# Kernel tuning notes

Measured on AMD Instinct MI355X. Metric: run time of the kernel, lower is better.

The kernel has to match this reference:

```python
import jax, jax.numpy as jnp
import numpy as np

K = 2            # top-k experts
TEMPERATURE = 1.0
EPS = 1e-9


def setup_inputs() -> dict:
    key = jax.random.key(0)
    k1, k2 = jax.random.split(key)
    B, S, D = 4, 4096, 4096
    G, E = 4, 64
    x = jax.random.normal(k1, (B, S, D), dtype=jnp.float32)
    # stacked gate weights, one [E, D] Linear weight per gate head
    W = jax.random.normal(k2, (G, E, D), dtype=jnp.float32) * 0.02
    return {"x": x, "W": W}


def reference(x, W):
    # per-head logits over experts: [B, S, G, E]; jitter disabled (eval / jitter_noise=0)
    logits = jnp.einsum('bsd,ged->bsge', x, W) * (1.0 / TEMPERATURE)
    probs = jax.nn.softmax(logits, axis=-1)          # softmax per head
    probs_full = probs.mean(axis=2)                  # consensus over heads: [B, S, E]
    topk_vals, idx = jax.lax.top_k(probs_full, K)    # sorted descending, matches aten.topk
    den = jnp.sum(topk_vals, axis=-1, keepdims=True)
    scores = topk_vals / jnp.maximum(den, EPS)       # clamp_min(den, 1e-9)
    pf = jax.lax.stop_gradient(probs_full)           # aux stats under no_grad
    importance = pf.mean(axis=(0, 1))                # [E]
    load = (pf > 0.0).astype(pf.dtype).mean(axis=(0, 1))  # [E]
    return idx, scores, probs_full, importance, load
```

## Files before the change

### kernel.cpp

```cpp
#include <hip/hip_runtime.h>

typedef _Float16 f16x8  __attribute__((ext_vector_type(8)));
typedef float    f32x4  __attribute__((ext_vector_type(4)));
typedef float    f32x16 __attribute__((ext_vector_type(16)));

#define MROWS 16384
#define NCOLS 256
#define KDIM  4096
#define BM    128
#define BK    32
#define LDA   34

#define OUT_SCORES 32768
#define OUT_PF     65536
#define OUT_IMP    1114112
#define OUT_LOAD   1114176

#define FIN_BLOCKS 1024

__global__ __launch_bounds__(256) void wprep(const float* __restrict__ W,
                                             _Float16* __restrict__ wfHi,
                                             _Float16* __restrict__ wfLo) {
    int t  = blockIdx.x * 256 + threadIdx.x;
    int n  = t >> 9;
    int k8 = t & 511;
    const float* src = W + ((size_t)n * KDIM + (size_t)k8 * 8);
    f16x8 hi, lo;
#pragma unroll
    for (int j = 0; j < 8; ++j) {
        float x = src[j];
        _Float16 h = (_Float16)x;
        hi[j] = h;
        lo[j] = (_Float16)(x - (float)h);
    }
    int NT    = n >> 5;
    int ksg   = k8 >> 2;
    int ksub  = (k8 >> 1) & 1;
    int lane  = (n & 31) + ((k8 & 1) << 5);
    size_t dst = ((size_t)((ksg * 8 + NT) * 2 + ksub) * 64 + (size_t)lane) * 8;
    *(f16x8*)(wfHi + dst) = hi;
    *(f16x8*)(wfLo + dst) = lo;
}

__global__ __launch_bounds__(256, 2) void gemm3(const float* __restrict__ X,
        const _Float16* __restrict__ wfHi, const _Float16* __restrict__ wfLo,
        float* __restrict__ lsplit, int kQ) {
    __shared__ _Float16 aHi[2][BM * LDA];
    __shared__ _Float16 aLo[2][BM * LDA];

    const int tid  = threadIdx.x;
    const int lane = tid & 63;
    const int w    = tid >> 6;
    const int mt   = blockIdx.x & 127;
    const int s    = blockIdx.x >> 7;
    const int m0   = mt * BM;
    const int k0   = s * kQ;
    const int iters = kQ / BK;

    f32x16 acc[4][2];
#pragma unroll
    for (int a = 0; a < 4; ++a)
#pragma unroll
        for (int b = 0; b < 2; ++b)
#pragma unroll
            for (int q = 0; q < 16; ++q) acc[a][b][q] = 0.f;

    const int sr = tid >> 1;
    const int sh = tid & 1;
    const float* xrow = X + ((size_t)(m0 + sr) * KDIM + (size_t)k0 + sh * 16);
    const int woff = sr * LDA + sh * 16;

    const int roff = (lane & 31) * LDA + (lane >> 5) * 8;

    size_t bbase = (size_t)(k0 >> 5) * 8192 + (size_t)(2 * w) * 1024 + (size_t)lane * 8;
    const _Float16* pBH = wfHi + bbase;
    const _Float16* pBL = wfLo + bbase;

    f32x4 xq[4];
#pragma unroll
    for (int q = 0; q < 4; ++q) xq[q] = *(const f32x4*)(xrow + q * 4);

    for (int i = 0; i < iters; ++i) {
        f16x8 bH[2][2], bL[2][2];
#pragma unroll
        for (int ni = 0; ni < 2; ++ni)
#pragma unroll
            for (int ks = 0; ks < 2; ++ks) {
                bH[ni][ks] = *(const f16x8*)(pBH + ni * 1024 + ks * 512);
                bL[ni][ks] = *(const f16x8*)(pBL + ni * 1024 + ks * 512);
            }
        pBH += 8192;
        pBL += 8192;

        f32x4 xqN[4];
        {
            const float* xp = xrow + (size_t)((i + 1 < iters) ? (i + 1) : 0) * BK;
#pragma unroll
            for (int q = 0; q < 4; ++q) xqN[q] = *(const f32x4*)(xp + q * 4);
        }

        float xv[16];
#pragma unroll
        for (int q = 0; q < 4; ++q) {
            xv[q*4+0] = xq[q][0]; xv[q*4+1] = xq[q][1];
            xv[q*4+2] = xq[q][2]; xv[q*4+3] = xq[q][3];
        }
        f16x8 h0, h1, l0, l1;
#pragma unroll
        for (int j = 0; j < 8; ++j) {
            _Float16 ha = (_Float16)xv[j];
            h0[j] = ha; l0[j] = (_Float16)(xv[j] - (float)ha);
            _Float16 hb = (_Float16)xv[8 + j];
            h1[j] = hb; l1[j] = (_Float16)(xv[8 + j] - (float)hb);
        }

        _Float16* wAH = &aHi[i & 1][woff];
        _Float16* wAL = &aLo[i & 1][woff];
        *(f16x8*)(wAH)     = h0;
        *(f16x8*)(wAH + 8) = h1;
        *(f16x8*)(wAL)     = l0;
        *(f16x8*)(wAL + 8) = l1;

        asm volatile("s_waitcnt lgkmcnt(0)" ::: "memory");
        __builtin_amdgcn_s_barrier();
        __builtin_amdgcn_sched_barrier(0);

        const _Float16* rAH = &aHi[i & 1][roff];
        const _Float16* rAL = &aLo[i & 1][roff];
        __builtin_amdgcn_s_setprio(1);
#pragma unroll
        for (int mi = 0; mi < 4; ++mi) {
            f16x8 aH0 = *(const f16x8*)(rAH + mi * 32 * LDA);
            f16x8 aH1 = *(const f16x8*)(rAH + mi * 32 * LDA + 16);
            f16x8 aL0 = *(const f16x8*)(rAL + mi * 32 * LDA);
            f16x8 aL1 = *(const f16x8*)(rAL + mi * 32 * LDA + 16);
#pragma unroll
            for (int ni = 0; ni < 2; ++ni) {
                acc[mi][ni] = __builtin_amdgcn_mfma_f32_32x32x16_f16(aH0, bH[ni][0], acc[mi][ni], 0, 0, 0);
                acc[mi][ni] = __builtin_amdgcn_mfma_f32_32x32x16_f16(aH1, bH[ni][1], acc[mi][ni], 0, 0, 0);
                acc[mi][ni] = __builtin_amdgcn_mfma_f32_32x32x16_f16(aH0, bL[ni][0], acc[mi][ni], 0, 0, 0);
                acc[mi][ni] = __builtin_amdgcn_mfma_f32_32x32x16_f16(aH1, bL[ni][1], acc[mi][ni], 0, 0, 0);
                acc[mi][ni] = __builtin_amdgcn_mfma_f32_32x32x16_f16(aL0, bH[ni][0], acc[mi][ni], 0, 0, 0);
                acc[mi][ni] = __builtin_amdgcn_mfma_f32_32x32x16_f16(aL1, bH[ni][1], acc[mi][ni], 0, 0, 0);
            }
        }
        __builtin_amdgcn_s_setprio(0);

#pragma unroll
        for (int q = 0; q < 4; ++q) xq[q] = xqN[q];
    }

    float* outp = lsplit + (size_t)s * ((size_t)MROWS * NCOLS);
#pragma unroll
    for (int mi = 0; mi < 4; ++mi) {
#pragma unroll
        for (int ni = 0; ni < 2; ++ni) {
            int col   = w * 64 + ni * 32 + (lane & 31);
            int rbase = m0 + mi * 32 + ((lane >> 5) << 2);
#pragma unroll
            for (int reg = 0; reg < 16; ++reg) {
                int row = rbase + (reg & 3) + ((reg >> 2) << 3);
                outp[(size_t)row * NCOLS + col] = acc[mi][ni][reg];
            }
        }
    }
}

__global__ __launch_bounds__(256) void finalize(const float* __restrict__ lsplit,
                                                int nsplit, float* __restrict__ out,
                                                float* __restrict__ paux) {
    __shared__ float sImp[64], sLoad[64];
    const int tid = threadIdx.x;
    if (tid < 64) { sImp[tid] = 0.f; sLoad[tid] = 0.f; }
    __syncthreads();

    const int i   = tid & 15;
    const int grp = tid >> 4;
    const int r   = blockIdx.x * 16 + grp;

    float v[16];
#pragma unroll
    for (int t = 0; t < 16; ++t) {
        size_t off = (size_t)r * 256 + (size_t)i + 16 * t;
        float a = lsplit[off];
        for (int s = 1; s < nsplit; ++s)
            a += lsplit[(size_t)s * ((size_t)MROWS * NCOLS) + off];
        v[t] = a;
    }

    float hm[4];
#pragma unroll
    for (int g = 0; g < 4; ++g) {
        float m = fmaxf(fmaxf(v[4*g], v[4*g+1]), fmaxf(v[4*g+2], v[4*g+3]));
#pragma unroll
        for (int msk = 1; msk < 16; msk <<= 1)
            m = fmaxf(m, __shfl_xor(m, msk));
        hm[g] = m;
    }
    float p[16], inv[4];
#pragma unroll
    for (int g = 0; g < 4; ++g) {
        float sa = 0.f;
#pragma unroll
        for (int q = 0; q < 4; ++q) { p[4*g+q] = __expf(v[4*g+q] - hm[g]); sa += p[4*g+q]; }
#pragma unroll
        for (int msk = 1; msk < 16; msk <<= 1)
            sa += __shfl_xor(sa, msk);
        inv[g] = 1.f / sa;
    }

    float pf[4];
#pragma unroll
    for (int et = 0; et < 4; ++et) {
        pf[et] = 0.25f * (p[et] * inv[0] + p[4+et] * inv[1] + p[8+et] * inv[2] + p[12+et] * inv[3]);
        out[OUT_PF + (size_t)r * 64 + i + 16 * et] = pf[et];
        atomicAdd(&sImp[i + 16 * et], pf[et]);
        atomicAdd(&sLoad[i + 16 * et], pf[et] > 0.f ? 1.f : 0.f);
    }

    float v1 = -3.4e38f, v2 = -3.4e38f; int e1 = 0, e2 = 0;
#pragma unroll
    for (int et = 0; et < 4; ++et) {
        int e = i + 16 * et; float val = pf[et];
        if (val > v1) { v2 = v1; e2 = e1; v1 = val; e1 = e; }
        else if (val > v2) { v2 = val; e2 = e; }
    }
#pragma unroll
    for (int msk = 1; msk < 16; msk <<= 1) {
        float o1 = __shfl_xor(v1, msk); int oe1 = __shfl_xor(e1, msk);
        float o2 = __shfl_xor(v2, msk); int oe2 = __shfl_xor(e2, msk);
        bool ob = (o1 > v1) || (o1 == v1 && oe1 < e1);
        if (ob) {
            bool vb = (v1 > o2) || (v1 == o2 && e1 < oe2);
            v2 = vb ? v1 : o2; e2 = vb ? e1 : oe2;
            v1 = o1; e1 = oe1;
        } else {
            bool nb = (o1 > v2) || (o1 == v2 && oe1 < e2);
            v2 = nb ? o1 : v2; e2 = nb ? oe1 : e2;
        }
    }
    if (i == 0) {
        float den = fmaxf(v1 + v2, 1e-9f);
        out[(size_t)r * 2]              = (float)e1;
        out[(size_t)r * 2 + 1]          = (float)e2;
        out[OUT_SCORES + (size_t)r * 2]     = v1 / den;
        out[OUT_SCORES + (size_t)r * 2 + 1] = v2 / den;
    }
    __syncthreads();
    if (tid < 128)
        paux[(size_t)blockIdx.x * 128 + tid] = (tid < 64) ? sImp[tid] : sLoad[tid - 64];
}

__global__ __launch_bounds__(1024) void reduce_aux(const float* __restrict__ paux,
                                                   float* __restrict__ out) {
    __shared__ float part[8][128];
    const int t = threadIdx.x & 127;
    const int g = threadIdx.x >> 7;
    float s = 0.f;
    for (int b = g * 128; b < g * 128 + 128; ++b)
        s += paux[(size_t)b * 128 + t];
    part[g][t] = s;
    __syncthreads();
    if (threadIdx.x < 128) {
        float a = 0.f;
#pragma unroll
        for (int g2 = 0; g2 < 8; ++g2) a += part[g2][t];
        out[OUT_IMP + t] = a * (1.0f / 16384.0f);
    }
}

extern "C" void kernel_launch(void* const* d_in, const int* in_sizes, int n_in,
                              void* d_out, int out_size, void* d_ws, size_t ws_size,
                              hipStream_t stream) {
    const float* X = (const float*)d_in[0];
    const float* W = (const float*)d_in[1];
    float* out = (float*)d_out;
    char* ws = (char*)d_ws;

    _Float16* wfHi = (_Float16*)ws;
    _Float16* wfLo = (_Float16*)(ws + (2u << 20));
    float* lsplit  = (float*)(ws + (4u << 20));

    const size_t per = 16u << 20;
    int nsplit = (ws_size >= (4u << 20) + 4 * per + (1u << 20)) ? 4
               : (ws_size >= (4u << 20) + 2 * per + (1u << 20)) ? 2 : 1;

    float* paux = (float*)(ws + (4u << 20) + (size_t)nsplit * per);

    wprep<<<512, 256, 0, stream>>>(W, wfHi, wfLo);
    gemm3<<<128 * nsplit, 256, 0, stream>>>(X, wfHi, wfLo, lsplit, KDIM / nsplit);
    finalize<<<FIN_BLOCKS, 256, 0, stream>>>(lsplit, nsplit, out, paux);
    reduce_aux<<<1, 1024, 0, stream>>>(paux, out);
}
```

Measured before the change: 494.4 us.

## Split GEMM block across 8 waves in a 2x4 grid with late B loads

The gemm kernel now runs 512 threads per block, with eight waves arranged 2x4 over the 128x256 tile. Each wave keeps half as many accumulators, which cuts register use and lets more waves sit on each CU (launch bounds 512,4). The A staging work is spread over four threads per row. B fragment loads move to after the barrier, computed from the iteration index. Moving those loads exposes their global-memory latency inside the MFMA phase, and every wave must still load the full B fragments for its columns.

Result: no change. 498.9 us (+0.9%).

```diff
diff --git a/kernel.cpp b/kernel.cpp
--- a/kernel.cpp
+++ b/kernel.cpp
@@ -42,7 +42,7 @@
     *(f16x8*)(wfLo + dst) = lo;
 }
 
-__global__ __launch_bounds__(256, 2) void gemm3(const float* __restrict__ X,
+__global__ __launch_bounds__(512, 4) void gemm3(const float* __restrict__ X,
         const _Float16* __restrict__ wfHi, const _Float16* __restrict__ wfLo,
         float* __restrict__ lsplit, int kQ) {
     __shared__ _Float16 aHi[2][BM * LDA];
@@ -51,85 +51,77 @@
     const int tid  = threadIdx.x;
     const int lane = tid & 63;
     const int w    = tid >> 6;
+    const int wr   = w >> 2;
+    const int wc   = w & 3;
     const int mt   = blockIdx.x & 127;
     const int s    = blockIdx.x >> 7;
     const int m0   = mt * BM;
     const int k0   = s * kQ;
     const int iters = kQ / BK;
 
-    f32x16 acc[4][2];
-#pragma unroll
-    for (int a = 0; a < 4; ++a)
+    f32x16 acc[2][2];
+#pragma unroll
+    for (int a = 0; a < 2; ++a)
 #pragma unroll
         for (int b = 0; b < 2; ++b)
 #pragma unroll
             for (int q = 0; q < 16; ++q) acc[a][b][q] = 0.f;
 
-    const int sr = tid >> 1;
-    const int sh = tid & 1;
-    const float* xrow = X + ((size_t)(m0 + sr) * KDIM + (size_t)k0 + sh * 16);
-    const int woff = sr * LDA + sh * 16;
-
-    const int roff = (lane & 31) * LDA + (lane >> 5) * 8;
-
-    size_t bbase = (size_t)(k0 >> 5) * 8192 + (size_t)(2 * w) * 1024 + (size_t)lane * 8;
-    const _Float16* pBH = wfHi + bbase;
-    const _Float16* pBL = wfLo + bbase;
-
-    f32x4 xq[4];
-#pragma unroll
-    for (int q = 0; q < 4; ++q) xq[q] = *(const f32x4*)(xrow + q * 4);
+    const int sr = tid >> 2;
+    const int sq = tid & 3;
+    const float* xrow = X + ((size_t)(m0 + sr) * KDIM + (size_t)k0 + sq * 8);
+    const int woff = sr * LDA + sq * 8;
+
+    const int roff = (wr * 64 + (lane & 31)) * LDA + (lane >> 5) * 8;
+
+    const size_t bbase = (size_t)(k0 >> 5) * 8192 + (size_t)(2 * wc) * 1024 + (size_t)lane * 8;
+    const _Float16* BH = wfHi + bbase;
+    const _Float16* BL = wfLo + bbase;
+
+    f32x4 xq0 = *(const f32x4*)(xrow);
+    f32x4 xq1 = *(const f32x4*)(xrow + 4);
 
     for (int i = 0; i < iters; ++i) {
-        f16x8 bH[2][2], bL[2][2];
-#pragma unroll
-        for (int ni = 0; ni < 2; ++ni)
-#pragma unroll
-            for (int ks = 0; ks < 2; ++ks) {
-                bH[ni][ks] = *(const f16x8*)(pBH + ni * 1024 + ks * 512);
-                bL[ni][ks] = *(const f16x8*)(pBL + ni * 1024 + ks * 512);
-            }
-        pBH += 8192;
-        pBL += 8192;
-
-        f32x4 xqN[4];
+        f32x4 xn0, xn1;
         {
             const float* xp = xrow + (size_t)((i + 1 < iters) ? (i + 1) : 0) * BK;
-#pragma unroll
-            for (int q = 0; q < 4; ++q) xqN[q] = *(const f32x4*)(xp + q * 4);
-        }
-
-        float xv[16];
-#pragma unroll
-        for (int q = 0; q < 4; ++q) {
-            xv[q*4+0] = xq[q][0]; xv[q*4+1] = xq[q][1];
-            xv[q*4+2] = xq[q][2]; xv[q*4+3] = xq[q][3];
-        }
-        f16x8 h0, h1, l0, l1;
+            xn0 = *(const f32x4*)(xp);
+            xn1 = *(const f32x4*)(xp + 4);
+        }
+
+        float xv[8];
+        xv[0] = xq0[0]; xv[1] = xq0[1]; xv[2] = xq0[2]; xv[3] = xq0[3];
+        xv[4] = xq1[0]; xv[5] = xq1[1]; xv[6] = xq1[2]; xv[7] = xq1[3];
+        f16x8 h, l;
 #pragma unroll
         for (int j = 0; j < 8; ++j) {
             _Float16 ha = (_Float16)xv[j];
-            h0[j] = ha; l0[j] = (_Float16)(xv[j] - (float)ha);
-            _Float16 hb = (_Float16)xv[8 + j];
-            h1[j] = hb; l1[j] = (_Float16)(xv[8 + j] - (float)hb);
-        }
-
-        _Float16* wAH = &aHi[i & 1][woff];
-        _Float16* wAL = &aLo[i & 1][woff];
-        *(f16x8*)(wAH)     = h0;
-        *(f16x8*)(wAH + 8) = h1;
-        *(f16x8*)(wAL)     = l0;
-        *(f16x8*)(wAL + 8) = l1;
+            h[j] = ha;
+            l[j] = (_Float16)(xv[j] - (float)ha);
+        }
+
+        *(f16x8*)(&aHi[i & 1][woff]) = h;
+        *(f16x8*)(&aLo[i & 1][woff]) = l;
 
         asm volatile("s_waitcnt lgkmcnt(0)" ::: "memory");
         __builtin_amdgcn_s_barrier();
         __builtin_amdgcn_sched_barrier(0);
 
+        f16x8 bH[2][2], bL[2][2];
+#pragma unroll
+        for (int ni = 0; ni < 2; ++ni)
+#pragma unroll
+            for (int ks = 0; ks < 2; ++ks) {
+                size_t off = (size_t)i * 8192 + (size_t)ni * 1024 + (size_t)ks * 512;
+                bH[ni][ks] = *(const f16x8*)(BH + off);
+                bL[ni][ks] = *(const f16x8*)(BL + off);
+            }
+
         const _Float16* rAH = &aHi[i & 1][roff];
         const _Float16* rAL = &aLo[i & 1][roff];
         __builtin_amdgcn_s_setprio(1);
 #pragma unroll
-        for (int mi = 0; mi < 4; ++mi) {
+        for (int mi = 0; mi < 2; ++mi) {
             f16x8 aH0 = *(const f16x8*)(rAH + mi * 32 * LDA);
             f16x8 aH1 = *(const f16x8*)(rAH + mi * 32 * LDA + 16);
             f16x8 aL0 = *(const f16x8*)(rAL + mi * 32 * LDA);
@@ -146,17 +138,16 @@
         }
         __builtin_amdgcn_s_setprio(0);
 
-#pragma unroll
-        for (int q = 0; q < 4; ++q) xq[q] = xqN[q];
+        xq0 = xn0; xq1 = xn1;
     }
 
     float* outp = lsplit + (size_t)s * ((size_t)MROWS * NCOLS);
 #pragma unroll
-    for (int mi = 0; mi < 4; ++mi) {
+    for (int mi = 0; mi < 2; ++mi) {
 #pragma unroll
         for (int ni = 0; ni < 2; ++ni) {
-            int col   = w * 64 + ni * 32 + (lane & 31);
-            int rbase = m0 + mi * 32 + ((lane >> 5) << 2);
+            int col   = wc * 64 + ni * 32 + (lane & 31);
+            int rbase = m0 + wr * 64 + mi * 32 + ((lane >> 5) << 2);
 #pragma unroll
             for (int reg = 0; reg < 16; ++reg) {
                 int row = rbase + (reg & 3) + ((reg >> 2) << 3);
@@ -288,7 +279,7 @@
     float* paux = (float*)(ws + (4u << 20) + (size_t)nsplit * per);
 
     wprep<<<512, 256, 0, stream>>>(W, wfHi, wfLo);
-    gemm3<<<128 * nsplit, 256, 0, stream>>>(X, wfHi, wfLo, lsplit, KDIM / nsplit);
+    gemm3<<<128 * nsplit, 512, 0, stream>>>(X, wfHi, wfLo, lsplit, KDIM / nsplit);
     finalize<<<FIN_BLOCKS, 256, 0, stream>>>(lsplit, nsplit, out, paux);
     reduce_aux<<<1, 1024, 0, stream>>>(paux, out);
 }
```
